# Optimization experiments

Measured on AMD Instinct MI355X. Metric: run time of the kernel, lower is better.

Reference implementation:

```python
import jax, jax.numpy as jnp
import numpy as np

HEADS = 8
DIM_HEAD = 64
DIM = 512
NUM_BANDS = 32
MAX_FREQ = 32.0
NORM_SCALE = 10.0
RPE_DIM = (NUM_BANDS * 2 + 1) * 2  # 130


def setup_inputs() -> dict:
    key = jax.random.key(0)
    ks = jax.random.split(key, 9)
    B, N = 2, 512
    inner = HEADS * DIM_HEAD
    h2 = HEADS * 2
    inp = {
        "x": jax.random.normal(ks[0], (B, N, DIM), dtype=jnp.float32),
        "positions": jax.random.uniform(ks[1], (B, N, 2), dtype=jnp.float32),
        "W_qkv": jax.random.normal(ks[2], (DIM, 3 * inner), dtype=jnp.float32) / np.sqrt(DIM),
        "W_out": jax.random.normal(ks[3], (inner, DIM), dtype=jnp.float32) / np.sqrt(inner),
        "b_out": jnp.zeros((DIM,), dtype=jnp.float32),
        "rpe_W1": jax.random.normal(ks[4], (RPE_DIM, h2), dtype=jnp.float32) / np.sqrt(RPE_DIM),
        "rpe_b1": jnp.zeros((h2,), dtype=jnp.float32),
        "rpe_W2": jax.random.normal(ks[5], (h2, HEADS), dtype=jnp.float32) / np.sqrt(h2),
        "rpe_b2": jnp.zeros((HEADS,), dtype=jnp.float32),
    }
    return inp


def _fourier_encode(x):
    # x: [...], returns [..., 2*NUM_BANDS+1]
    freqs = jnp.linspace(1.0, MAX_FREQ, NUM_BANDS, dtype=x.dtype)
    angles = x[..., None] * freqs * jnp.pi
    return jnp.concatenate([x[..., None], jnp.sin(angles), jnp.cos(angles)], axis=-1)


def _rpe_bias(positions, W1, b1, W2, b2):
    # positions: [B, N, 2] -> bias [B, H, N, N]
    delta = positions[:, None, :, :] - positions[:, :, None, :]  # key_pos_j - query_pos_i
    dx = delta[..., 0] / NORM_SCALE
    dy = delta[..., 1] / NORM_SCALE
    dx = dx / (1.0 + jnp.abs(dx))
    dy = dy / (1.0 + jnp.abs(dy))
    feats = jnp.concatenate([_fourier_encode(dx), _fourier_encode(dy)], axis=-1)  # [B,N,N,130]
    h = jax.nn.gelu(feats @ W1 + b1, approximate=False)
    bias = h @ W2 + b2  # [B, N, N, H]
    return jnp.transpose(bias, (0, 3, 1, 2))  # [B, H, N, N]


def reference(x, positions, W_qkv, W_out, b_out, rpe_W1, rpe_b1, rpe_W2, rpe_b2):
    B, N, _ = x.shape
    H, d = HEADS, DIM_HEAD
    scale = d ** (-0.5)
    qkv = x @ W_qkv  # [B, N, 3*H*d]
    q, k, v = jnp.split(qkv, 3, axis=-1)
    q = q.reshape(B, N, H, d)
    k = k.reshape(B, N, H, d)
    v = v.reshape(B, N, H, d)
    scores = jnp.einsum('bihd,bjhd->bhij', q, k) * scale
    scores = scores + _rpe_bias(positions, rpe_W1, rpe_b1, rpe_W2, rpe_b2)
    attn = jax.nn.softmax(scores, axis=-1)
    out = jnp.einsum('bhij,bjhd->bihd', attn, v).reshape(B, N, H * d)
    return out @ W_out + b_out
```

## Files before the change

### kernel.cpp

```cpp
#include <hip/hip_runtime.h>
#include <hip/hip_fp16.h>
#include <math.h>

typedef __attribute__((ext_vector_type(8))) _Float16 f16x8;
typedef __attribute__((ext_vector_type(4))) float f32x4;

#define TBL 512
#define UMAXV (1.0f/11.0f)

__device__ __forceinline__ int swq(int row, int q) {
  return row * 64 + ((q ^ (row & 7)) << 3);
}
__device__ __forceinline__ f16x8 cvt8(float4 a, float4 b) {
  f16x8 r;
  r[0] = (_Float16)a.x; r[1] = (_Float16)a.y;
  r[2] = (_Float16)a.z; r[3] = (_Float16)a.w;
  r[4] = (_Float16)b.x; r[5] = (_Float16)b.y;
  r[6] = (_Float16)b.z; r[7] = (_Float16)b.w;
  return r;
}

__global__ __launch_bounds__(256) void k_prep(
    const float* __restrict__ Wqkv, const float* __restrict__ Wout,
    const float* __restrict__ W1, const float* __restrict__ b1,
    _Float16* __restrict__ Wt, _Float16* __restrict__ Wot,
    __half* __restrict__ Tx, __half* __restrict__ Ty) {
  __shared__ float Tt[32 * 33];
  const int t = threadIdx.x;
  const int bid = blockIdx.x;
  if (bid >= 1024) {
    int gid = (bid - 1024) * 256 + t;
    int e = gid >> 5, c = gid & 31;
    float u = -UMAXV + (2.0f * UMAXV) * (float)e / (float)(TBL - 1);
    const int xpart = (c < 16);
    const int col = c & 15;
    const int base = xpart ? 0 : 65;
    float sum = u * W1[base * 16 + col] + (xpart ? b1[col] : 0.0f);
    float s1, c1;
    sincosf(u * 3.14159265358979323846f, &s1, &c1);
    float sk = s1, ck = c1;
    for (int k = 1; k <= 32; ++k) {
      sum += sk * W1[(base + k) * 16 + col] + ck * W1[(base + 32 + k) * 16 + col];
      float ns = sk * c1 + ck * s1;
      ck = ck * c1 - sk * s1;
      sk = ns;
    }
    (xpart ? Tx : Ty)[e * 16 + col] = __float2half(sum);
    return;
  }
  int k0, n0, ncols;
  const float* W;
  _Float16* O;
  if (bid < 768) {
    k0 = (bid / 48) * 32; n0 = (bid % 48) * 32; ncols = 1536;
    W = Wqkv; O = Wt;
  } else {
    int tile = bid - 768;
    k0 = (tile / 16) * 32; n0 = (tile % 16) * 32; ncols = 512;
    W = Wout; O = Wot;
  }
  {
    int kl = t >> 3, nl = (t & 7) * 4;
    float4 v = *(const float4*)&W[(k0 + kl) * ncols + n0 + nl];
    Tt[kl * 33 + nl + 0] = v.x;
    Tt[kl * 33 + nl + 1] = v.y;
    Tt[kl * 33 + nl + 2] = v.z;
    Tt[kl * 33 + nl + 3] = v.w;
  }
  __syncthreads();
  {
    int nl = t >> 3, kq = (t & 7) * 4;
    ushort4 h;
    h.x = __builtin_bit_cast(unsigned short, (_Float16)Tt[(kq + 0) * 33 + nl]);
    h.y = __builtin_bit_cast(unsigned short, (_Float16)Tt[(kq + 1) * 33 + nl]);
    h.z = __builtin_bit_cast(unsigned short, (_Float16)Tt[(kq + 2) * 33 + nl]);
    h.w = __builtin_bit_cast(unsigned short, (_Float16)Tt[(kq + 3) * 33 + nl]);
    *(ushort4*)&O[(n0 + nl) * 512 + k0 + kq] = h;
  }
}

__global__ __launch_bounds__(512) void k_fused(
    const float* __restrict__ x, const _Float16* __restrict__ Wt,
    _Float16* __restrict__ q16, _Float16* __restrict__ k16,
    _Float16* __restrict__ vt16,
    const float* __restrict__ pos,
    const __half* __restrict__ Tx, const __half* __restrict__ Ty,
    const float* __restrict__ W2, const float* __restrict__ b2,
    _Float16* __restrict__ bias) {
  __shared__ __align__(16) unsigned short SM[16384];
  const int bid = blockIdx.x;
  const int t = threadIdx.x;

  if (bid < 192) {
    _Float16* Ah = (_Float16*)SM;
    _Float16* Bh = (_Float16*)SM + 8192;
    const int mt = bid / 24, nt = bid % 24;
    const int m0 = mt * 128, n0 = nt * 64;
    const int w = t >> 6, lane = t & 63, blk = lane >> 4, jc = lane & 15;
    const int mw = (w & 3) * 32, nw = (w >> 2) * 32;
    const int sa = t >> 3, sq = t & 7;

    f32x4 acc[2][2];
    #pragma unroll
    for (int i = 0; i < 2; ++i)
      #pragma unroll
      for (int j = 0; j < 2; ++j) acc[i][j] = f32x4{0.f, 0.f, 0.f, 0.f};

    float4 pax[2][2];
    f16x8 pbv;
    #pragma unroll
    for (int c = 0; c < 2; ++c) {
      const float* xp = &x[(m0 + sa + c * 64) * 512 + sq * 8];
      pax[c][0] = *(const float4*)xp;
      pax[c][1] = *(const float4*)(xp + 4);
    }
    pbv = *(const f16x8*)&Wt[(n0 + sa) * 512 + sq * 8];

    for (int it = 0; it < 8; ++it) {
      #pragma unroll
      for (int c = 0; c < 2; ++c)
        *(f16x8*)&Ah[swq(sa + c * 64, sq)] = cvt8(pax[c][0], pax[c][1]);
      *(f16x8*)&Bh[swq(sa, sq)] = pbv;
      __syncthreads();
      if (it < 7) {
        int k0 = (it + 1) * 64;
        #pragma unroll
        for (int c = 0; c < 2; ++c) {
          const float* xp = &x[(m0 + sa + c * 64) * 512 + k0 + sq * 8];
          pax[c][0] = *(const float4*)xp;
          pax[c][1] = *(const float4*)(xp + 4);
        }
        pbv = *(const f16x8*)&Wt[(n0 + sa) * 512 + k0 + sq * 8];
      }
      #pragma unroll
      for (int h = 0; h < 2; ++h) {
        int q = h * 4 + blk;
        f16x8 a0 = *(const f16x8*)&Ah[swq(mw + jc, q)];
        f16x8 a1 = *(const f16x8*)&Ah[swq(mw + 16 + jc, q)];
        f16x8 b0 = *(const f16x8*)&Bh[swq(nw + jc, q)];
        f16x8 b1 = *(const f16x8*)&Bh[swq(nw + 16 + jc, q)];
        acc[0][0] = __builtin_amdgcn_mfma_f32_16x16x32_f16(a0, b0, acc[0][0], 0, 0, 0);
        acc[0][1] = __builtin_amdgcn_mfma_f32_16x16x32_f16(a0, b1, acc[0][1], 0, 0, 0);
        acc[1][0] = __builtin_amdgcn_mfma_f32_16x16x32_f16(a1, b0, acc[1][0], 0, 0, 0);
        acc[1][1] = __builtin_amdgcn_mfma_f32_16x16x32_f16(a1, b1, acc[1][1], 0, 0, 0);
      }
      __syncthreads();
    }
    const int sec = n0 >> 9;
    const int hh_ = (n0 >> 6) & 7;
    if (sec < 2) {
      _Float16* dst = (sec == 0) ? q16 : k16;
      const float scl = (sec == 0) ? 0.125f : 1.0f;
      #pragma unroll
      for (int i = 0; i < 2; ++i)
        #pragma unroll
        for (int j = 0; j < 2; ++j)
          #pragma unroll
          for (int r = 0; r < 4; ++r) {
            int tok = m0 + mw + i * 16 + blk * 4 + r;
            int b = tok >> 9, nn = tok & 511;
            int d = nw + j * 16 + jc;
            dst[((b * 8 + hh_) * 512 + nn) * 64 + d] = (_Float16)(acc[i][j][r] * scl);
          }
    } else {
      _Float16* T = (_Float16*)SM;
      #pragma unroll
      for (int i = 0; i < 2; ++i)
        #pragma unroll
        for (int j = 0; j < 2; ++j)
          #pragma unroll
          for (int r = 0; r < 4; ++r)
            T[(nw + j * 16 + jc) * 136 + mw + i * 16 + blk * 4 + r] =
                (_Float16)acc[i][j][r];
      __syncthreads();
      const int d = t >> 3, tq = t & 7;
      const int b = m0 >> 9, nb = m0 & 511;
      #pragma unroll
      for (int c = 0; c < 2; ++c) {
        int qd = tq + c * 8;
        f16x8 vv = *(const f16x8*)&T[d * 136 + qd * 8];
        *(f16x8*)&vt16[((b * 8 + hh_) * 64 + d) * 512 + nb + qd * 8] = vv;
      }
    }
    return;
  }

  const int gid = (bid - 192) * 512 + t;
  const int b = gid >> 18;
  const int i = (gid >> 9) & 511;
  const int j = gid & 511;
  const float pix = pos[(b * 512 + i) * 2 + 0];
  const float piy = pos[(b * 512 + i) * 2 + 1];
  const float pjx = pos[(b * 512 + j) * 2 + 0];
  const float pjy = pos[(b * 512 + j) * 2 + 1];
  float txv = (pjx - pix) * 0.1f; float ux = txv / (1.0f + fabsf(txv));
  float tyv = (pjy - piy) * 0.1f; float uy = tyv / (1.0f + fabsf(tyv));
  const float invstep = (float)(TBL - 1) / (2.0f * UMAXV);
  float fx = (ux + UMAXV) * invstep;
  int ix = (int)fx; ix = min(max(ix, 0), TBL - 2);
  float wx = fx - (float)ix;
  float fy = (uy + UMAXV) * invstep;
  int iy = (int)fy; iy = min(max(iy, 0), TBL - 2);
  float wy = fy - (float)iy;

  __half hx0[16], hx1[16], hy0[16], hy1[16];
  *(uint4*)&hx0[0] = *(const uint4*)&Tx[ix * 16];
  *(uint4*)&hx0[8] = *(const uint4*)&Tx[ix * 16 + 8];
  *(uint4*)&hx1[0] = *(const uint4*)&Tx[(ix + 1) * 16];
  *(uint4*)&hx1[8] = *(const uint4*)&Tx[(ix + 1) * 16 + 8];
  *(uint4*)&hy0[0] = *(const uint4*)&Ty[iy * 16];
  *(uint4*)&hy0[8] = *(const uint4*)&Ty[iy * 16 + 8];
  *(uint4*)&hy1[0] = *(const uint4*)&Ty[(iy + 1) * 16];
  *(uint4*)&hy1[8] = *(const uint4*)&Ty[(iy + 1) * 16 + 8];

  float o[8];
  #pragma unroll
  for (int c = 0; c < 8; ++c) o[c] = b2[c];
  #pragma unroll
  for (int r = 0; r < 16; ++r) {
    float ax = __half2float(hx0[r]);
    float bx = __half2float(hx1[r]);
    float ay = __half2float(hy0[r]);
    float by = __half2float(hy1[r]);
    float hv = fmaf(wx, bx - ax, ax) + fmaf(wy, by - ay, ay);
    float z = hv * 0.70710678118654752f;
    float az = fabsf(z);
    float tt = __builtin_amdgcn_rcpf(fmaf(0.3275911f, az, 1.0f));
    float poly = ((((1.061405429f * tt - 1.453152027f) * tt + 1.421413741f) * tt
                   - 0.284496736f) * tt + 0.254829592f) * tt;
    float ex = __expf(-z * z);
    float erfv = copysignf(fmaf(-poly, ex, 1.0f), z);
    float g = 0.5f * hv * (1.0f + erfv);
    #pragma unroll
    for (int c = 0; c < 8; ++c)
      o[c] = fmaf(g, W2[r * 8 + c], o[c]);
  }
  #pragma unroll
  for (int c = 0; c < 8; ++c)
    bias[((size_t)(b * 8 + c) * 512 + i) * 512 + j] = (_Float16)o[c];
}

__global__ __launch_bounds__(512) void k_attn(
    const _Float16* __restrict__ q16, const _Float16* __restrict__ k16,
    const _Float16* __restrict__ vt16, const _Float16* __restrict__ bias,
    _Float16* __restrict__ ao16) {
  __shared__ __align__(16) _Float16 psu[8 * 512];
  __shared__ __align__(16) float olds[8 * 16 * 65];
  __shared__ float mls[8 * 16 * 2];
  _Float16* bst = (_Float16*)olds;

  const int bid = blockIdx.x;
  const int it = bid & 31, h = (bid >> 5) & 7, b = bid >> 8;
  const int i0 = it * 16;
  const int bh = b * 8 + h;
  const int tid = threadIdx.x;
  const int w = tid >> 6, lane = tid & 63;
  const int blk = lane >> 4, jc = lane & 15;

  {
    const _Float16* bgp = bias + ((size_t)(bh * 512 + i0)) * 512;
    int brow = tid >> 5, bc = (tid & 31) * 16;
    *(f16x8*)&bst[brow * 520 + bc]     = *(const f16x8*)&bgp[brow * 512 + bc];
    *(f16x8*)&bst[brow * 520 + bc + 8] = *(const f16x8*)&bgp[brow * 512 + bc + 8];
  }

  const int qoff = (bh * 512 + i0 + jc) * 64 + blk * 8;
  const f16x8 qa0 = *(const f16x8*)&q16[qoff];
  const f16x8 qa1 = *(const f16x8*)&q16[qoff + 32];

  float m[4] = {-1e30f, -1e30f, -1e30f, -1e30f};
  float l[4] = {0.f, 0.f, 0.f, 0.f};
  f32x4 o[4];
  #pragma unroll
  for (int dt = 0; dt < 4; ++dt) o[dt] = f32x4{0.f, 0.f, 0.f, 0.f};

  _Float16* pw = &psu[w * 512];
  __syncthreads();

  #pragma unroll
  for (int jt = 0; jt < 2; ++jt) {
    const int j0 = w * 64 + jt * 32;
    const int rA = (bh * 512 + j0 + jc) * 64 + blk * 8;
    const int rB = rA + 16 * 64;
    f16x8 kA0 = *(const f16x8*)&k16[rA];
    f16x8 kA1 = *(const f16x8*)&k16[rA + 32];
    f16x8 kB0 = *(const f16x8*)&k16[rB];
    f16x8 kB1 = *(const f16x8*)&k16[rB + 32];

    f32x4 aA = {0.f, 0.f, 0.f, 0.f};
    aA = __builtin_amdgcn_mfma_f32_16x16x32_f16(qa0, kA0, aA, 0, 0, 0);
    aA = __builtin_amdgcn_mfma_f32_16x16x32_f16(qa1, kA1, aA, 0, 0, 0);
    f32x4 aB = {0.f, 0.f, 0.f, 0.f};
    aB = __builtin_amdgcn_mfma_f32_16x16x32_f16(qa0, kB0, aB, 0, 0, 0);
    aB = __builtin_amdgcn_mfma_f32_16x16x32_f16(qa1, kB1, aB, 0, 0, 0);

    float sA[4], sB[4], sc[4];
    #pragma unroll
    for (int r = 0; r < 4; ++r) {
      const int br = (blk * 4 + r) * 520;
      sA[r] = aA[r] + (float)bst[br + j0 + jc];
      sB[r] = aB[r] + (float)bst[br + j0 + 16 + jc];
    }
    #pragma unroll
    for (int r = 0; r < 4; ++r) {
      float mx = fmaxf(sA[r], sB[r]);
      mx = fmaxf(mx, __shfl_xor(mx, 1, 64));
      mx = fmaxf(mx, __shfl_xor(mx, 2, 64));
      mx = fmaxf(mx, __shfl_xor(mx, 4, 64));
      mx = fmaxf(mx, __shfl_xor(mx, 8, 64));
      float mn = fmaxf(m[r], mx);
      sc[r] = __expf(m[r] - mn);
      m[r] = mn;
      float pA = __expf(sA[r] - mn);
      float pB = __expf(sB[r] - mn);
      float ps = pA + pB;
      ps += __shfl_xor(ps, 1, 64);
      ps += __shfl_xor(ps, 2, 64);
      ps += __shfl_xor(ps, 4, 64);
      ps += __shfl_xor(ps, 8, 64);
      l[r] = l[r] * sc[r] + ps;
      pw[(blk * 4 + r) * 32 + jc] = (_Float16)pA;
      pw[(blk * 4 + r) * 32 + 16 + jc] = (_Float16)pB;
    }
    #pragma unroll
    for (int dt = 0; dt < 4; ++dt)
      #pragma unroll
      for (int r = 0; r < 4; ++r)
        o[dt][r] *= sc[r];
    f16x8 pf = *(const f16x8*)&pw[jc * 32 + blk * 8];
    #pragma unroll
    for (int dt = 0; dt < 4; ++dt) {
      const int va = (bh * 64 + dt * 16 + jc) * 512 + j0 + blk * 8;
      f16x8 vh = *(const f16x8*)&vt16[va];
      o[dt] = __builtin_amdgcn_mfma_f32_16x16x32_f16(pf, vh, o[dt], 0, 0, 0);
    }
  }
  __syncthreads();
  #pragma unroll
  for (int dt = 0; dt < 4; ++dt)
    #pragma unroll
    for (int r = 0; r < 4; ++r)
      olds[(w * 16 + blk * 4 + r) * 65 + dt * 16 + jc] = o[dt][r];
  if (jc == 0) {
    #pragma unroll
    for (int r = 0; r < 4; ++r) {
      mls[(w * 16 + blk * 4 + r) * 2 + 0] = m[r];
      mls[(w * 16 + blk * 4 + r) * 2 + 1] = l[r];
    }
  }
  __syncthreads();
  #pragma unroll
  for (int itx = 0; itx < 2; ++itx) {
    int idx = tid + itx * 512;
    int q = idx >> 6, d = idx & 63;
    float M = -1e30f;
    #pragma unroll
    for (int ww = 0; ww < 8; ++ww) M = fmaxf(M, mls[(ww * 16 + q) * 2]);
    float L = 0.f, acc = 0.f;
    #pragma unroll
    for (int ww = 0; ww < 8; ++ww) {
      float e = __expf(mls[(ww * 16 + q) * 2] - M);
      L += mls[(ww * 16 + q) * 2 + 1] * e;
      acc += olds[(ww * 16 + q) * 65 + d] * e;
    }
    ao16[(b * 512 + i0 + q) * 512 + h * 64 + d] = (_Float16)(acc / L);
  }
}

__global__ __launch_bounds__(256) void k_out(
    const _Float16* __restrict__ ao16, const _Float16* __restrict__ Wot,
    const float* __restrict__ bout, float* __restrict__ out) {
  __shared__ __align__(16) unsigned short SM[6144];
  _Float16* Ah = (_Float16*)SM;
  _Float16* Bh = (_Float16*)SM + 2048;

  const int bid = blockIdx.x;
  const int mt = bid >> 3, nt = bid & 7;
  const int m0 = mt * 32, n0 = nt * 64;
  const int t = threadIdx.x;
  const int w = t >> 6, lane = t & 63, blk = lane >> 4, jc = lane & 15;
  const int mh_ = (w & 1) * 16, nh_ = (w >> 1) * 32;
  const int sm = t >> 3, sq = t & 7;

  f32x4 acc[2];
  acc[0] = f32x4{0.f, 0.f, 0.f, 0.f};
  acc[1] = f32x4{0.f, 0.f, 0.f, 0.f};

  f16x8 pa, pb[2];
  {
    pa = *(const f16x8*)&ao16[(m0 + sm) * 512 + sq * 8];
    #pragma unroll
    for (int c = 0; c < 2; ++c)
      pb[c] = *(const f16x8*)&Wot[(n0 + sm + c * 32) * 512 + sq * 8];
  }
  for (int it = 0; it < 8; ++it) {
    *(f16x8*)&Ah[swq(sm, sq)] = pa;
    #pragma unroll
    for (int c = 0; c < 2; ++c)
      *(f16x8*)&Bh[swq(sm + c * 32, sq)] = pb[c];
    __syncthreads();
    if (it < 7) {
      int k0 = (it + 1) * 64;
      pa = *(const f16x8*)&ao16[(m0 + sm) * 512 + k0 + sq * 8];
      #pragma unroll
      for (int c = 0; c < 2; ++c)
        pb[c] = *(const f16x8*)&Wot[(n0 + sm + c * 32) * 512 + k0 + sq * 8];
    }
    #pragma unroll
    for (int h = 0; h < 2; ++h) {
      int q = h * 4 + blk;
      f16x8 a0 = *(const f16x8*)&Ah[swq(mh_ + jc, q)];
      f16x8 b0 = *(const f16x8*)&Bh[swq(nh_ + jc, q)];
      f16x8 b1 = *(const f16x8*)&Bh[swq(nh_ + 16 + jc, q)];
      acc[0] = __builtin_amdgcn_mfma_f32_16x16x32_f16(a0, b0, acc[0], 0, 0, 0);
      acc[1] = __builtin_amdgcn_mfma_f32_16x16x32_f16(a0, b1, acc[1], 0, 0, 0);
    }
    __syncthreads();
  }
  #pragma unroll
  for (int j = 0; j < 2; ++j) {
    int n = n0 + nh_ + j * 16 + jc;
    float bb = bout[n];
    #pragma unroll
    for (int r = 0; r < 4; ++r) {
      int row = m0 + mh_ + blk * 4 + r;
      out[row * 512 + n] = acc[j][r] + bb;
    }
  }
}

extern "C" void kernel_launch(void* const* d_in, const int* in_sizes, int n_in,
                              void* d_out, int out_size, void* d_ws, size_t ws_size,
                              hipStream_t stream) {
  const float* x    = (const float*)d_in[0];
  const float* pos  = (const float*)d_in[1];
  const float* Wqkv = (const float*)d_in[2];
  const float* Wout = (const float*)d_in[3];
  const float* bout = (const float*)d_in[4];
  const float* W1   = (const float*)d_in[5];
  const float* b1   = (const float*)d_in[6];
  const float* W2   = (const float*)d_in[7];
  const float* b2   = (const float*)d_in[8];
  float* out = (float*)d_out;
  char* base = (char*)d_ws;

  __half* Tx       = (__half*)(base);
  __half* Ty       = (__half*)(base + 16384);
  _Float16* Wt     = (_Float16*)(base + 32768);
  _Float16* Wot    = (_Float16*)(base + 1605632);
  _Float16* q16    = (_Float16*)(base + 2129920);
  _Float16* k16    = (_Float16*)(base + 3178496);
  _Float16* vt16   = (_Float16*)(base + 4227072);
  _Float16* bias16 = (_Float16*)(base + 5275648);
  _Float16* ao16   = (_Float16*)(base + 13664256);

  hipLaunchKernelGGL(k_prep, dim3(1088), dim3(256), 0, stream,
                     Wqkv, Wout, W1, b1, Wt, Wot, Tx, Ty);
  hipLaunchKernelGGL(k_fused, dim3(1216), dim3(512), 0, stream,
                     x, Wt, q16, k16, vt16, pos, Tx, Ty, W2, b2, bias16);
  hipLaunchKernelGGL(k_attn, dim3(512), dim3(512), 0, stream,
                     q16, k16, vt16, bias16, ao16);
  hipLaunchKernelGGL(k_out, dim3(256), dim3(256), 0, stream,
                     ao16, Wot, bout, out);
}
```

Before: 43.97 us.

## Prefetch all K-tiles into registers and double-buffer LDS in GEMM and attention kernels

The QKV projection and output-projection GEMMs now issue every global load for all eight K-steps up front into registers, then use two LDS buffers so only one barrier per step is needed. The attention kernel hoists all K and V fragment loads ahead of the softmax loop. The aim is to expose more memory-level parallelism and hide global load latency. In exchange, register pressure rises sharply (e.g. 32 float4 per thread in the fused kernel) and LDS use grows, which may lower occupancy or cause spills.

New measurement: 46.56 us. 1.06x slower.

```diff
diff --git a/kernel.cpp b/kernel.cpp
--- a/kernel.cpp
+++ b/kernel.cpp
@@ -87,13 +87,13 @@
     const __half* __restrict__ Tx, const __half* __restrict__ Ty,
     const float* __restrict__ W2, const float* __restrict__ b2,
     _Float16* __restrict__ bias) {
-  __shared__ __align__(16) unsigned short SM[16384];
+  __shared__ __align__(16) char SMEM[49152];
   const int bid = blockIdx.x;
   const int t = threadIdx.x;
 
   if (bid < 192) {
-    _Float16* Ah = (_Float16*)SM;
-    _Float16* Bh = (_Float16*)SM + 8192;
+    _Float16* Ah[2] = {(_Float16*)SMEM, (_Float16*)SMEM + 12288};
+    _Float16* Bh[2] = {(_Float16*)SMEM + 8192, (_Float16*)SMEM + 20480};
     const int mt = bid / 24, nt = bid % 24;
     const int m0 = mt * 128, n0 = nt * 64;
     const int w = t >> 6, lane = t & 63, blk = lane >> 4, jc = lane & 15;
@@ -106,39 +106,41 @@
       #pragma unroll
       for (int j = 0; j < 2; ++j) acc[i][j] = f32x4{0.f, 0.f, 0.f, 0.f};
 
-    float4 pax[2][2];
-    f16x8 pbv;
-    #pragma unroll
-    for (int c = 0; c < 2; ++c) {
-      const float* xp = &x[(m0 + sa + c * 64) * 512 + sq * 8];
-      pax[c][0] = *(const float4*)xp;
-      pax[c][1] = *(const float4*)(xp + 4);
-    }
-    pbv = *(const f16x8*)&Wt[(n0 + sa) * 512 + sq * 8];
-
+    float4 pax[8][2][2];
+    f16x8 pbv[8];
+    #pragma unroll
     for (int it = 0; it < 8; ++it) {
       #pragma unroll
-      for (int c = 0; c < 2; ++c)
-        *(f16x8*)&Ah[swq(sa + c * 64, sq)] = cvt8(pax[c][0], pax[c][1]);
-      *(f16x8*)&Bh[swq(sa, sq)] = pbv;
-      __syncthreads();
+      for (int c = 0; c < 2; ++c) {
+        const float* xp = &x[(m0 + sa + c * 64) * 512 + it * 64 + sq * 8];
+        pax[it][c][0] = *(const float4*)xp;
+        pax[it][c][1] = *(const float4*)(xp + 4);
+      }
+      pbv[it] = *(const f16x8*)&Wt[(n0 + sa) * 512 + it * 64 + sq * 8];
+    }
+    #pragma unroll
+    for (int c = 0; c < 2; ++c)
+      *(f16x8*)&Ah[0][swq(sa + c * 64, sq)] = cvt8(pax[0][c][0], pax[0][c][1]);
+    *(f16x8*)&Bh[0][swq(sa, sq)] = pbv[0];
+    __syncthreads();
+
+    #pragma unroll
+    for (int it = 0; it < 8; ++it) {
+      const int cur = it & 1, nxt = cur ^ 1;
       if (it < 7) {
-        int k0 = (it + 1) * 64;
         #pragma unroll
-        for (int c = 0; c < 2; ++c) {
-          const float* xp = &x[(m0 + sa + c * 64) * 512 + k0 + sq * 8];
-          pax[c][0] = *(const float4*)xp;
-          pax[c][1] = *(const float4*)(xp + 4);
-        }
-        pbv = *(const f16x8*)&Wt[(n0 + sa) * 512 + k0 + sq * 8];
+        for (int c = 0; c < 2; ++c)
+          *(f16x8*)&Ah[nxt][swq(sa + c * 64, sq)] =
+              cvt8(pax[it + 1][c][0], pax[it + 1][c][1]);
+        *(f16x8*)&Bh[nxt][swq(sa, sq)] = pbv[it + 1];
       }
       #pragma unroll
       for (int h = 0; h < 2; ++h) {
         int q = h * 4 + blk;
-        f16x8 a0 = *(const f16x8*)&Ah[swq(mw + jc, q)];
-        f16x8 a1 = *(const f16x8*)&Ah[swq(mw + 16 + jc, q)];
-        f16x8 b0 = *(const f16x8*)&Bh[swq(nw + jc, q)];
-        f16x8 b1 = *(const f16x8*)&Bh[swq(nw + 16 + jc, q)];
+        f16x8 a0 = *(const f16x8*)&Ah[cur][swq(mw + jc, q)];
+        f16x8 a1 = *(const f16x8*)&Ah[cur][swq(mw + 16 + jc, q)];
+        f16x8 b0 = *(const f16x8*)&Bh[cur][swq(nw + jc, q)];
+        f16x8 b1 = *(const f16x8*)&Bh[cur][swq(nw + 16 + jc, q)];
         acc[0][0] = __builtin_amdgcn_mfma_f32_16x16x32_f16(a0, b0, acc[0][0], 0, 0, 0);
         acc[0][1] = __builtin_amdgcn_mfma_f32_16x16x32_f16(a0, b1, acc[0][1], 0, 0, 0);
         acc[1][0] = __builtin_amdgcn_mfma_f32_16x16x32_f16(a1, b0, acc[1][0], 0, 0, 0);
@@ -163,7 +165,7 @@
             dst[((b * 8 + hh_) * 512 + nn) * 64 + d] = (_Float16)(acc[i][j][r] * scl);
           }
     } else {
-      _Float16* T = (_Float16*)SM;
+      _Float16* T = (_Float16*)SMEM;
       #pragma unroll
       for (int i = 0; i < 2; ++i)
         #pragma unroll
@@ -268,31 +270,39 @@
   const f16x8 qa0 = *(const f16x8*)&q16[qoff];
   const f16x8 qa1 = *(const f16x8*)&q16[qoff + 32];
 
-  float m[4] = {-1e30f, -1e30f, -1e30f, -1e30f};
-  float l[4] = {0.f, 0.f, 0.f, 0.f};
-  f32x4 o[4];
-  #pragma unroll
-  for (int dt = 0; dt < 4; ++dt) o[dt] = f32x4{0.f, 0.f, 0.f, 0.f};
-
-  _Float16* pw = &psu[w * 512];
-  __syncthreads();
-
+  f16x8 kf[2][4], vf[2][4];
   #pragma unroll
   for (int jt = 0; jt < 2; ++jt) {
     const int j0 = w * 64 + jt * 32;
     const int rA = (bh * 512 + j0 + jc) * 64 + blk * 8;
     const int rB = rA + 16 * 64;
-    f16x8 kA0 = *(const f16x8*)&k16[rA];
-    f16x8 kA1 = *(const f16x8*)&k16[rA + 32];
-    f16x8 kB0 = *(const f16x8*)&k16[rB];
-    f16x8 kB1 = *(const f16x8*)&k16[rB + 32];
-
+    kf[jt][0] = *(const f16x8*)&k16[rA];
+    kf[jt][1] = *(const f16x8*)&k16[rA + 32];
+    kf[jt][2] = *(const f16x8*)&k16[rB];
+    kf[jt][3] = *(const f16x8*)&k16[rB + 32];
+    #pragma unroll
+    for (int dt = 0; dt < 4; ++dt)
+      vf[jt][dt] = *(const f16x8*)&vt16[(bh * 64 + dt * 16 + jc) * 512 + j0 + blk * 8];
+  }
+
+  float m[4] = {-1e30f, -1e30f, -1e30f, -1e30f};
+  float l[4] = {0.f, 0.f, 0.f, 0.f};
+  f32x4 o[4];
+  #pragma unroll
+  for (int dt = 0; dt < 4; ++dt) o[dt] = f32x4{0.f, 0.f, 0.f, 0.f};
+
+  _Float16* pw = &psu[w * 512];
+  __syncthreads();
+
+  #pragma unroll
+  for (int jt = 0; jt < 2; ++jt) {
+    const int j0 = w * 64 + jt * 32;
     f32x4 aA = {0.f, 0.f, 0.f, 0.f};
-    aA = __builtin_amdgcn_mfma_f32_16x16x32_f16(qa0, kA0, aA, 0, 0, 0);
-    aA = __builtin_amdgcn_mfma_f32_16x16x32_f16(qa1, kA1, aA, 0, 0, 0);
+    aA = __builtin_amdgcn_mfma_f32_16x16x32_f16(qa0, kf[jt][0], aA, 0, 0, 0);
+    aA = __builtin_amdgcn_mfma_f32_16x16x32_f16(qa1, kf[jt][1], aA, 0, 0, 0);
     f32x4 aB = {0.f, 0.f, 0.f, 0.f};
-    aB = __builtin_amdgcn_mfma_f32_16x16x32_f16(qa0, kB0, aB, 0, 0, 0);
-    aB = __builtin_amdgcn_mfma_f32_16x16x32_f16(qa1, kB1, aB, 0, 0, 0);
+    aB = __builtin_amdgcn_mfma_f32_16x16x32_f16(qa0, kf[jt][2], aB, 0, 0, 0);
+    aB = __builtin_amdgcn_mfma_f32_16x16x32_f16(qa1, kf[jt][3], aB, 0, 0, 0);
 
     float sA[4], sB[4], sc[4];
     #pragma unroll
@@ -329,11 +339,8 @@
         o[dt][r] *= sc[r];
     f16x8 pf = *(const f16x8*)&pw[jc * 32 + blk * 8];
     #pragma unroll
-    for (int dt = 0; dt < 4; ++dt) {
-      const int va = (bh * 64 + dt * 16 + jc) * 512 + j0 + blk * 8;
-      f16x8 vh = *(const f16x8*)&vt16[va];
-      o[dt] = __builtin_amdgcn_mfma_f32_16x16x32_f16(pf, vh, o[dt], 0, 0, 0);
-    }
+    for (int dt = 0; dt < 4; ++dt)
+      o[dt] = __builtin_amdgcn_mfma_f32_16x16x32_f16(pf, vf[jt][dt], o[dt], 0, 0, 0);
   }
   __syncthreads();
   #pragma unroll
@@ -370,9 +377,9 @@
 __global__ __launch_bounds__(256) void k_out(
     const _Float16* __restrict__ ao16, const _Float16* __restrict__ Wot,
     const float* __restrict__ bout, float* __restrict__ out) {
-  __shared__ __align__(16) unsigned short SM[6144];
-  _Float16* Ah = (_Float16*)SM;
-  _Float16* Bh = (_Float16*)SM + 2048;
+  __shared__ __align__(16) char SMEM[24576];
+  _Float16* Ah[2] = {(_Float16*)SMEM, (_Float16*)SMEM + 6144};
+  _Float16* Bh[2] = {(_Float16*)SMEM + 2048, (_Float16*)SMEM + 8192};
 
   const int bid = blockIdx.x;
   const int mt = bid >> 3, nt = bid & 7;
@@ -386,32 +393,35 @@
   acc[0] = f32x4{0.f, 0.f, 0.f, 0.f};
   acc[1] = f32x4{0.f, 0.f, 0.f, 0.f};
 
-  f16x8 pa, pb[2];
-  {
-    pa = *(const f16x8*)&ao16[(m0 + sm) * 512 + sq * 8];
+  f16x8 pa[8], pb[8][2];
+  #pragma unroll
+  for (int it = 0; it < 8; ++it) {
+    pa[it] = *(const f16x8*)&ao16[(m0 + sm) * 512 + it * 64 + sq * 8];
     #pragma unroll
     for (int c = 0; c < 2; ++c)
-      pb[c] = *(const f16x8*)&Wot[(n0 + sm + c * 32) * 512 + sq * 8];
-  }
+      pb[it][c] = *(const f16x8*)&Wot[(n0 + sm + c * 32) * 512 + it * 64 + sq * 8];
+  }
+  *(f16x8*)&Ah[0][swq(sm, sq)] = pa[0];
+  #pragma unroll
+  for (int c = 0; c < 2; ++c)
+    *(f16x8*)&Bh[0][swq(sm + c * 32, sq)] = pb[0][c];
+  __syncthreads();
+
+  #pragma unroll
   for (int it = 0; it < 8; ++it) {
-    *(f16x8*)&Ah[swq(sm, sq)] = pa;
-    #pragma unroll
-    for (int c = 0; c < 2; ++c)
-      *(f16x8*)&Bh[swq(sm + c * 32, sq)] = pb[c];
-    __syncthreads();
+    const int cur = it & 1, nxt = cur ^ 1;
     if (it < 7) {
-      int k0 = (it + 1) * 64;
-      pa = *(const f16x8*)&ao16[(m0 + sm) * 512 + k0 + sq * 8];
+      *(f16x8*)&Ah[nxt][swq(sm, sq)] = pa[it + 1];
       #pragma unroll
       for (int c = 0; c < 2; ++c)
-        pb[c] = *(const f16x8*)&Wot[(n0 + sm + c * 32) * 512 + k0 + sq * 8];
+        *(f16x8*)&Bh[nxt][swq(sm + c * 32, sq)] = pb[it + 1][c];
     }
     #pragma unroll
     for (int h = 0; h < 2; ++h) {
       int q = h * 4 + blk;
-      f16x8 a0 = *(const f16x8*)&Ah[swq(mh_ + jc, q)];
-      f16x8 b0 = *(const f16x8*)&Bh[swq(nh_ + jc, q)];
-      f16x8 b1 = *(const f16x8*)&Bh[swq(nh_ + 16 + jc, q)];
+      f16x8 a0 = *(const f16x8*)&Ah[cur][swq(mh_ + jc, q)];
+      f16x8 b0 = *(const f16x8*)&Bh[cur][swq(nh_ + jc, q)];
+      f16x8 b1 = *(const f16x8*)&Bh[cur][swq(nh_ + 16 + jc, q)];
       acc[0] = __builtin_amdgcn_mfma_f32_16x16x32_f16(a0, b0, acc[0], 0, 0, 0);
       acc[1] = __builtin_amdgcn_mfma_f32_16x16x32_f16(a0, b1, acc[1], 0, 0, 0);
     }
```

## Fuse attention with output projection, one wave per head over full key range

Applied to the files above, without the earlier changes.

Replaces the separate attention and output-projection kernels with one kernel. Each block now handles a 16-query tile for all 8 heads, one wave per head, and each wave loops over all 512 keys itself, so the cross-wave softmax merge is gone. The normalized head outputs are kept in swizzled shared memory and multiplied by W_out in the same block, which removes the ao16 round trip through global memory and one launch. The cost is a grid of only 64 blocks on a many-CU GPU and a longer serial key loop per wave, so parallelism drops sharply.

After: 72.35 us. 64.5% more time.

```diff
diff --git a/kernel.cpp b/kernel.cpp
--- a/kernel.cpp
+++ b/kernel.cpp
@@ -240,29 +240,22 @@
     bias[((size_t)(b * 8 + c) * 512 + i) * 512 + j] = (_Float16)o[c];
 }
 
-__global__ __launch_bounds__(512) void k_attn(
+__global__ __launch_bounds__(512) void k_attn2(
     const _Float16* __restrict__ q16, const _Float16* __restrict__ k16,
     const _Float16* __restrict__ vt16, const _Float16* __restrict__ bias,
-    _Float16* __restrict__ ao16) {
+    const _Float16* __restrict__ Wot, const float* __restrict__ bout,
+    float* __restrict__ out) {
   __shared__ __align__(16) _Float16 psu[8 * 512];
-  __shared__ __align__(16) float olds[8 * 16 * 65];
-  __shared__ float mls[8 * 16 * 2];
-  _Float16* bst = (_Float16*)olds;
+  __shared__ __align__(16) _Float16 bstw[8 * 512];
+  __shared__ __align__(16) _Float16 aos[16 * 512];
 
   const int bid = blockIdx.x;
-  const int it = bid & 31, h = (bid >> 5) & 7, b = bid >> 8;
+  const int it = bid & 31, b = bid >> 5;
   const int i0 = it * 16;
-  const int bh = b * 8 + h;
   const int tid = threadIdx.x;
   const int w = tid >> 6, lane = tid & 63;
   const int blk = lane >> 4, jc = lane & 15;
-
-  {
-    const _Float16* bgp = bias + ((size_t)(bh * 512 + i0)) * 512;
-    int brow = tid >> 5, bc = (tid & 31) * 16;
-    *(f16x8*)&bst[brow * 520 + bc]     = *(const f16x8*)&bgp[brow * 512 + bc];
-    *(f16x8*)&bst[brow * 520 + bc + 8] = *(const f16x8*)&bgp[brow * 512 + bc + 8];
-  }
+  const int bh = b * 8 + w;
 
   const int qoff = (bh * 512 + i0 + jc) * 64 + blk * 8;
   const f16x8 qa0 = *(const f16x8*)&q16[qoff];
@@ -275,11 +268,14 @@
   for (int dt = 0; dt < 4; ++dt) o[dt] = f32x4{0.f, 0.f, 0.f, 0.f};
 
   _Float16* pw = &psu[w * 512];
-  __syncthreads();
-
-  #pragma unroll
-  for (int jt = 0; jt < 2; ++jt) {
-    const int j0 = w * 64 + jt * 32;
+  _Float16* bw = &bstw[w * 512];
+  const int brow = lane >> 2, bcol = (lane & 3) * 8;
+  const _Float16* bgp = bias + ((size_t)(bh * 512 + i0)) * 512;
+
+  for (int js = 0; js < 16; ++js) {
+    const int j0 = js * 32;
+    *(f16x8*)&bw[brow * 32 + bcol] = *(const f16x8*)&bgp[brow * 512 + j0 + bcol];
+
     const int rA = (bh * 512 + j0 + jc) * 64 + blk * 8;
     const int rB = rA + 16 * 64;
     f16x8 kA0 = *(const f16x8*)&k16[rA];
@@ -297,9 +293,9 @@
     float sA[4], sB[4], sc[4];
     #pragma unroll
     for (int r = 0; r < 4; ++r) {
-      const int br = (blk * 4 + r) * 520;
-      sA[r] = aA[r] + (float)bst[br + j0 + jc];
-      sB[r] = aB[r] + (float)bst[br + j0 + 16 + jc];
+      const int br = (blk * 4 + r) * 32;
+      sA[r] = aA[r] + (float)bw[br + jc];
+      sB[r] = aB[r] + (float)bw[br + 16 + jc];
     }
     #pragma unroll
     for (int r = 0; r < 4; ++r) {
@@ -330,101 +326,46 @@
     f16x8 pf = *(const f16x8*)&pw[jc * 32 + blk * 8];
     #pragma unroll
     for (int dt = 0; dt < 4; ++dt) {
-      const int va = (bh * 64 + dt * 16 + jc) * 512 + j0 + blk * 8;
-      f16x8 vh = *(const f16x8*)&vt16[va];
+      const f16x8 vh = *(const f16x8*)&vt16[(bh * 64 + dt * 16 + jc) * 512 + j0 + blk * 8];
       o[dt] = __builtin_amdgcn_mfma_f32_16x16x32_f16(pf, vh, o[dt], 0, 0, 0);
     }
   }
+
+  float inv[4];
+  #pragma unroll
+  for (int r = 0; r < 4; ++r) inv[r] = 1.0f / l[r];
+  #pragma unroll
+  for (int dt = 0; dt < 4; ++dt)
+    #pragma unroll
+    for (int r = 0; r < 4; ++r) {
+      int row = blk * 4 + r;
+      int col = w * 64 + dt * 16 + jc;
+      aos[row * 512 + (((col >> 3) ^ (row & 7)) << 3) + (col & 7)] =
+          (_Float16)(o[dt][r] * inv[r]);
+    }
   __syncthreads();
-  #pragma unroll
-  for (int dt = 0; dt < 4; ++dt)
-    #pragma unroll
-    for (int r = 0; r < 4; ++r)
-      olds[(w * 16 + blk * 4 + r) * 65 + dt * 16 + jc] = o[dt][r];
-  if (jc == 0) {
+
+  f32x4 acc[4];
+  #pragma unroll
+  for (int ns = 0; ns < 4; ++ns) acc[ns] = f32x4{0.f, 0.f, 0.f, 0.f};
+  #pragma unroll
+  for (int ks = 0; ks < 16; ++ks) {
+    const f16x8 af = *(const f16x8*)&aos[jc * 512 + (((ks * 4 + blk) ^ (jc & 7)) << 3)];
+    #pragma unroll
+    for (int ns = 0; ns < 4; ++ns) {
+      const f16x8 bf =
+          *(const f16x8*)&Wot[(w * 64 + ns * 16 + jc) * 512 + ks * 32 + blk * 8];
+      acc[ns] = __builtin_amdgcn_mfma_f32_16x16x32_f16(af, bf, acc[ns], 0, 0, 0);
+    }
+  }
+  #pragma unroll
+  for (int ns = 0; ns < 4; ++ns) {
+    int n = w * 64 + ns * 16 + jc;
+    float bb = bout[n];
     #pragma unroll
     for (int r = 0; r < 4; ++r) {
-      mls[(w * 16 + blk * 4 + r) * 2 + 0] = m[r];
-      mls[(w * 16 + blk * 4 + r) * 2 + 1] = l[r];
-    }
-  }
-  __syncthreads();
-  #pragma unroll
-  for (int itx = 0; itx < 2; ++itx) {
-    int idx = tid + itx * 512;
-    int q = idx >> 6, d = idx & 63;
-    float M = -1e30f;
-    #pragma unroll
-    for (int ww = 0; ww < 8; ++ww) M = fmaxf(M, mls[(ww * 16 + q) * 2]);
-    float L = 0.f, acc = 0.f;
-    #pragma unroll
-    for (int ww = 0; ww < 8; ++ww) {
-      float e = __expf(mls[(ww * 16 + q) * 2] - M);
-      L += mls[(ww * 16 + q) * 2 + 1] * e;
-      acc += olds[(ww * 16 + q) * 65 + d] * e;
-    }
-    ao16[(b * 512 + i0 + q) * 512 + h * 64 + d] = (_Float16)(acc / L);
-  }
-}
-
-__global__ __launch_bounds__(256) void k_out(
-    const _Float16* __restrict__ ao16, const _Float16* __restrict__ Wot,
-    const float* __restrict__ bout, float* __restrict__ out) {
-  __shared__ __align__(16) unsigned short SM[6144];
-  _Float16* Ah = (_Float16*)SM;
-  _Float16* Bh = (_Float16*)SM + 2048;
-
-  const int bid = blockIdx.x;
-  const int mt = bid >> 3, nt = bid & 7;
-  const int m0 = mt * 32, n0 = nt * 64;
-  const int t = threadIdx.x;
-  const int w = t >> 6, lane = t & 63, blk = lane >> 4, jc = lane & 15;
-  const int mh_ = (w & 1) * 16, nh_ = (w >> 1) * 32;
-  const int sm = t >> 3, sq = t & 7;
-
-  f32x4 acc[2];
-  acc[0] = f32x4{0.f, 0.f, 0.f, 0.f};
-  acc[1] = f32x4{0.f, 0.f, 0.f, 0.f};
-
-  f16x8 pa, pb[2];
-  {
-    pa = *(const f16x8*)&ao16[(m0 + sm) * 512 + sq * 8];
-    #pragma unroll
-    for (int c = 0; c < 2; ++c)
-      pb[c] = *(const f16x8*)&Wot[(n0 + sm + c * 32) * 512 + sq * 8];
-  }
-  for (int it = 0; it < 8; ++it) {
-    *(f16x8*)&Ah[swq(sm, sq)] = pa;
-    #pragma unroll
-    for (int c = 0; c < 2; ++c)
-      *(f16x8*)&Bh[swq(sm + c * 32, sq)] = pb[c];
-    __syncthreads();
-    if (it < 7) {
-      int k0 = (it + 1) * 64;
-      pa = *(const f16x8*)&ao16[(m0 + sm) * 512 + k0 + sq * 8];
-      #pragma unroll
-      for (int c = 0; c < 2; ++c)
-        pb[c] = *(const f16x8*)&Wot[(n0 + sm + c * 32) * 512 + k0 + sq * 8];
-    }
-    #pragma unroll
-    for (int h = 0; h < 2; ++h) {
-      int q = h * 4 + blk;
-      f16x8 a0 = *(const f16x8*)&Ah[swq(mh_ + jc, q)];
-      f16x8 b0 = *(const f16x8*)&Bh[swq(nh_ + jc, q)];
-      f16x8 b1 = *(const f16x8*)&Bh[swq(nh_ + 16 + jc, q)];
-      acc[0] = __builtin_amdgcn_mfma_f32_16x16x32_f16(a0, b0, acc[0], 0, 0, 0);
-      acc[1] = __builtin_amdgcn_mfma_f32_16x16x32_f16(a0, b1, acc[1], 0, 0, 0);
-    }
-    __syncthreads();
-  }
-  #pragma unroll
-  for (int j = 0; j < 2; ++j) {
-    int n = n0 + nh_ + j * 16 + jc;
-    float bb = bout[n];
-    #pragma unroll
-    for (int r = 0; r < 4; ++r) {
-      int row = m0 + mh_ + blk * 4 + r;
-      out[row * 512 + n] = acc[j][r] + bb;
+      int row = i0 + blk * 4 + r;
+      out[(b * 512 + row) * 512 + n] = acc[ns][r] + bb;
     }
   }
 }
@@ -452,14 +393,11 @@
   _Float16* k16    = (_Float16*)(base + 3178496);
   _Float16* vt16   = (_Float16*)(base + 4227072);
   _Float16* bias16 = (_Float16*)(base + 5275648);
-  _Float16* ao16   = (_Float16*)(base + 13664256);
 
   hipLaunchKernelGGL(k_prep, dim3(1088), dim3(256), 0, stream,
                      Wqkv, Wout, W1, b1, Wt, Wot, Tx, Ty);
   hipLaunchKernelGGL(k_fused, dim3(1216), dim3(512), 0, stream,
                      x, Wt, q16, k16, vt16, pos, Tx, Ty, W2, b2, bias16);
-  hipLaunchKernelGGL(k_attn, dim3(512), dim3(512), 0, stream,
-                     q16, k16, vt16, bias16, ao16);
-  hipLaunchKernelGGL(k_out, dim3(256), dim3(256), 0, stream,
-                     ao16, Wot, bout, out);
-}
+  hipLaunchKernelGGL(k_attn2, dim3(64), dim3(512), 0, stream,
+                     q16, k16, vt16, bias16, Wot, bout, out);
+}
```

## Deepen register prefetch to two stages and remap block order for XCD locality

Applied to the files above, without the earlier changes.

The QKV GEMM and output-projection GEMM now prefetch two k-tiles ahead into registers instead of one, aiming to hide global load latency. The attention kernel's two-tile loop is unrolled by hand so the K and V loads for both tiles are issued early, ahead of the MFMA and softmax work. All three kernels remap blockIdx so consecutive logical tiles are spread across groups of eight, presumably to place related tiles on the same XCD for L2 reuse. The cost is higher register pressure, which may lower occupancy.

Measured after the change: 43.14 us, median of 2. Within noise of the previous version (-1.9%).

```diff
diff --git a/kernel.cpp b/kernel.cpp
--- a/kernel.cpp
+++ b/kernel.cpp
@@ -92,9 +92,10 @@
   const int t = threadIdx.x;
 
   if (bid < 192) {
+    const int gb = (bid & 7) * 24 + (bid >> 3);
     _Float16* Ah = (_Float16*)SM;
     _Float16* Bh = (_Float16*)SM + 8192;
-    const int mt = bid / 24, nt = bid % 24;
+    const int mt = gb / 24, nt = gb % 24;
     const int m0 = mt * 128, n0 = nt * 64;
     const int w = t >> 6, lane = t & 63, blk = lane >> 4, jc = lane & 15;
     const int mw = (w & 3) * 32, nw = (w >> 2) * 32;
@@ -106,31 +107,35 @@
       #pragma unroll
       for (int j = 0; j < 2; ++j) acc[i][j] = f32x4{0.f, 0.f, 0.f, 0.f};
 
-    float4 pax[2][2];
-    f16x8 pbv;
-    #pragma unroll
-    for (int c = 0; c < 2; ++c) {
-      const float* xp = &x[(m0 + sa + c * 64) * 512 + sq * 8];
-      pax[c][0] = *(const float4*)xp;
-      pax[c][1] = *(const float4*)(xp + 4);
-    }
-    pbv = *(const f16x8*)&Wt[(n0 + sa) * 512 + sq * 8];
+    float4 pax[2][2][2];
+    f16x8 pbv[2];
+    #pragma unroll
+    for (int s = 0; s < 2; ++s) {
+      #pragma unroll
+      for (int c = 0; c < 2; ++c) {
+        const float* xp = &x[(m0 + sa + c * 64) * 512 + s * 64 + sq * 8];
+        pax[s][c][0] = *(const float4*)xp;
+        pax[s][c][1] = *(const float4*)(xp + 4);
+      }
+      pbv[s] = *(const f16x8*)&Wt[(n0 + sa) * 512 + s * 64 + sq * 8];
+    }
 
     for (int it = 0; it < 8; ++it) {
+      const int slot = it & 1;
       #pragma unroll
       for (int c = 0; c < 2; ++c)
-        *(f16x8*)&Ah[swq(sa + c * 64, sq)] = cvt8(pax[c][0], pax[c][1]);
-      *(f16x8*)&Bh[swq(sa, sq)] = pbv;
+        *(f16x8*)&Ah[swq(sa + c * 64, sq)] = cvt8(pax[slot][c][0], pax[slot][c][1]);
+      *(f16x8*)&Bh[swq(sa, sq)] = pbv[slot];
       __syncthreads();
-      if (it < 7) {
-        int k0 = (it + 1) * 64;
+      if (it < 6) {
+        int k0 = (it + 2) * 64;
         #pragma unroll
         for (int c = 0; c < 2; ++c) {
           const float* xp = &x[(m0 + sa + c * 64) * 512 + k0 + sq * 8];
-          pax[c][0] = *(const float4*)xp;
-          pax[c][1] = *(const float4*)(xp + 4);
+          pax[slot][c][0] = *(const float4*)xp;
+          pax[slot][c][1] = *(const float4*)(xp + 4);
         }
-        pbv = *(const f16x8*)&Wt[(n0 + sa) * 512 + k0 + sq * 8];
+        pbv[slot] = *(const f16x8*)&Wt[(n0 + sa) * 512 + k0 + sq * 8];
       }
       #pragma unroll
       for (int h = 0; h < 2; ++h) {
@@ -249,8 +254,8 @@
   __shared__ float mls[8 * 16 * 2];
   _Float16* bst = (_Float16*)olds;
 
-  const int bid = blockIdx.x;
-  const int it = bid & 31, h = (bid >> 5) & 7, b = bid >> 8;
+  const int lb = (blockIdx.x & 7) * 64 + (blockIdx.x >> 3);
+  const int it = lb & 31, h = (lb >> 5) & 7, b = lb >> 8;
   const int i0 = it * 16;
   const int bh = b * 8 + h;
   const int tid = threadIdx.x;
@@ -268,6 +273,20 @@
   const f16x8 qa0 = *(const f16x8*)&q16[qoff];
   const f16x8 qa1 = *(const f16x8*)&q16[qoff + 32];
 
+  const int j00 = w * 64;
+  f16x8 k0A0, k0A1, k0B0, k0B1, v0[4];
+  {
+    const int rA = (bh * 512 + j00 + jc) * 64 + blk * 8;
+    const int rB = rA + 16 * 64;
+    k0A0 = *(const f16x8*)&k16[rA];
+    k0A1 = *(const f16x8*)&k16[rA + 32];
+    k0B0 = *(const f16x8*)&k16[rB];
+    k0B1 = *(const f16x8*)&k16[rB + 32];
+    #pragma unroll
+    for (int dt = 0; dt < 4; ++dt)
+      v0[dt] = *(const f16x8*)&vt16[(bh * 64 + dt * 16 + jc) * 512 + j00 + blk * 8];
+  }
+
   float m[4] = {-1e30f, -1e30f, -1e30f, -1e30f};
   float l[4] = {0.f, 0.f, 0.f, 0.f};
   f32x4 o[4];
@@ -277,29 +296,34 @@
   _Float16* pw = &psu[w * 512];
   __syncthreads();
 
-  #pragma unroll
-  for (int jt = 0; jt < 2; ++jt) {
-    const int j0 = w * 64 + jt * 32;
-    const int rA = (bh * 512 + j0 + jc) * 64 + blk * 8;
+  f32x4 aA = {0.f, 0.f, 0.f, 0.f};
+  aA = __builtin_amdgcn_mfma_f32_16x16x32_f16(qa0, k0A0, aA, 0, 0, 0);
+  aA = __builtin_amdgcn_mfma_f32_16x16x32_f16(qa1, k0A1, aA, 0, 0, 0);
+  f32x4 aB = {0.f, 0.f, 0.f, 0.f};
+  aB = __builtin_amdgcn_mfma_f32_16x16x32_f16(qa0, k0B0, aB, 0, 0, 0);
+  aB = __builtin_amdgcn_mfma_f32_16x16x32_f16(qa1, k0B1, aB, 0, 0, 0);
+
+  const int j01 = w * 64 + 32;
+  f16x8 k1A0, k1A1, k1B0, k1B1, v1[4];
+  {
+    const int rA = (bh * 512 + j01 + jc) * 64 + blk * 8;
     const int rB = rA + 16 * 64;
-    f16x8 kA0 = *(const f16x8*)&k16[rA];
-    f16x8 kA1 = *(const f16x8*)&k16[rA + 32];
-    f16x8 kB0 = *(const f16x8*)&k16[rB];
-    f16x8 kB1 = *(const f16x8*)&k16[rB + 32];
-
-    f32x4 aA = {0.f, 0.f, 0.f, 0.f};
-    aA = __builtin_amdgcn_mfma_f32_16x16x32_f16(qa0, kA0, aA, 0, 0, 0);
-    aA = __builtin_amdgcn_mfma_f32_16x16x32_f16(qa1, kA1, aA, 0, 0, 0);
-    f32x4 aB = {0.f, 0.f, 0.f, 0.f};
-    aB = __builtin_amdgcn_mfma_f32_16x16x32_f16(qa0, kB0, aB, 0, 0, 0);
-    aB = __builtin_amdgcn_mfma_f32_16x16x32_f16(qa1, kB1, aB, 0, 0, 0);
-
+    k1A0 = *(const f16x8*)&k16[rA];
+    k1A1 = *(const f16x8*)&k16[rA + 32];
+    k1B0 = *(const f16x8*)&k16[rB];
+    k1B1 = *(const f16x8*)&k16[rB + 32];
+    #pragma unroll
+    for (int dt = 0; dt < 4; ++dt)
+      v1[dt] = *(const f16x8*)&vt16[(bh * 64 + dt * 16 + jc) * 512 + j01 + blk * 8];
+  }
+
+  {
     float sA[4], sB[4], sc[4];
     #pragma unroll
     for (int r = 0; r < 4; ++r) {
       const int br = (blk * 4 + r) * 520;
-      sA[r] = aA[r] + (float)bst[br + j0 + jc];
-      sB[r] = aB[r] + (float)bst[br + j0 + 16 + jc];
+      sA[r] = aA[r] + (float)bst[br + j00 + jc];
+      sB[r] = aB[r] + (float)bst[br + j00 + 16 + jc];
     }
     #pragma unroll
     for (int r = 0; r < 4; ++r) {
@@ -329,12 +353,56 @@
         o[dt][r] *= sc[r];
     f16x8 pf = *(const f16x8*)&pw[jc * 32 + blk * 8];
     #pragma unroll
-    for (int dt = 0; dt < 4; ++dt) {
-      const int va = (bh * 64 + dt * 16 + jc) * 512 + j0 + blk * 8;
-      f16x8 vh = *(const f16x8*)&vt16[va];
-      o[dt] = __builtin_amdgcn_mfma_f32_16x16x32_f16(pf, vh, o[dt], 0, 0, 0);
-    }
-  }
+    for (int dt = 0; dt < 4; ++dt)
+      o[dt] = __builtin_amdgcn_mfma_f32_16x16x32_f16(pf, v0[dt], o[dt], 0, 0, 0);
+  }
+
+  aA = f32x4{0.f, 0.f, 0.f, 0.f};
+  aA = __builtin_amdgcn_mfma_f32_16x16x32_f16(qa0, k1A0, aA, 0, 0, 0);
+  aA = __builtin_amdgcn_mfma_f32_16x16x32_f16(qa1, k1A1, aA, 0, 0, 0);
+  aB = f32x4{0.f, 0.f, 0.f, 0.f};
+  aB = __builtin_amdgcn_mfma_f32_16x16x32_f16(qa0, k1B0, aB, 0, 0, 0);
+  aB = __builtin_amdgcn_mfma_f32_16x16x32_f16(qa1, k1B1, aB, 0, 0, 0);
+  {
+    float sA[4], sB[4], sc[4];
+    #pragma unroll
+    for (int r = 0; r < 4; ++r) {
+      const int br = (blk * 4 + r) * 520;
+      sA[r] = aA[r] + (float)bst[br + j01 + jc];
+      sB[r] = aB[r] + (float)bst[br + j01 + 16 + jc];
+    }
+    #pragma unroll
+    for (int r = 0; r < 4; ++r) {
+      float mx = fmaxf(sA[r], sB[r]);
+      mx = fmaxf(mx, __shfl_xor(mx, 1, 64));
+      mx = fmaxf(mx, __shfl_xor(mx, 2, 64));
+      mx = fmaxf(mx, __shfl_xor(mx, 4, 64));
+      mx = fmaxf(mx, __shfl_xor(mx, 8, 64));
+      float mn = fmaxf(m[r], mx);
+      sc[r] = __expf(m[r] - mn);
+      m[r] = mn;
+      float pA = __expf(sA[r] - mn);
+      float pB = __expf(sB[r] - mn);
+      float ps = pA + pB;
+      ps += __shfl_xor(ps, 1, 64);
+      ps += __shfl_xor(ps, 2, 64);
+      ps += __shfl_xor(ps, 4, 64);
+      ps += __shfl_xor(ps, 8, 64);
+      l[r] = l[r] * sc[r] + ps;
+      pw[(blk * 4 + r) * 32 + jc] = (_Float16)pA;
+      pw[(blk * 4 + r) * 32 + 16 + jc] = (_Float16)pB;
+    }
+    #pragma unroll
+    for (int dt = 0; dt < 4; ++dt)
+      #pragma unroll
+      for (int r = 0; r < 4; ++r)
+        o[dt][r] *= sc[r];
+    f16x8 pf = *(const f16x8*)&pw[jc * 32 + blk * 8];
+    #pragma unroll
+    for (int dt = 0; dt < 4; ++dt)
+      o[dt] = __builtin_amdgcn_mfma_f32_16x16x32_f16(pf, v1[dt], o[dt], 0, 0, 0);
+  }
+
   __syncthreads();
   #pragma unroll
   for (int dt = 0; dt < 4; ++dt)
@@ -374,8 +442,8 @@
   _Float16* Ah = (_Float16*)SM;
   _Float16* Bh = (_Float16*)SM + 2048;
 
-  const int bid = blockIdx.x;
-  const int mt = bid >> 3, nt = bid & 7;
+  const int lb = (blockIdx.x & 7) * 32 + (blockIdx.x >> 3);
+  const int mt = lb >> 3, nt = lb & 7;
   const int m0 = mt * 32, n0 = nt * 64;
   const int t = threadIdx.x;
   const int w = t >> 6, lane = t & 63, blk = lane >> 4, jc = lane & 15;
@@ -386,25 +454,27 @@
   acc[0] = f32x4{0.f, 0.f, 0.f, 0.f};
   acc[1] = f32x4{0.f, 0.f, 0.f, 0.f};
 
-  f16x8 pa, pb[2];
-  {
-    pa = *(const f16x8*)&ao16[(m0 + sm) * 512 + sq * 8];
+  f16x8 pa[2], pb[2][2];
+  #pragma unroll
+  for (int s = 0; s < 2; ++s) {
+    pa[s] = *(const f16x8*)&ao16[(m0 + sm) * 512 + s * 64 + sq * 8];
     #pragma unroll
     for (int c = 0; c < 2; ++c)
-      pb[c] = *(const f16x8*)&Wot[(n0 + sm + c * 32) * 512 + sq * 8];
+      pb[s][c] = *(const f16x8*)&Wot[(n0 + sm + c * 32) * 512 + s * 64 + sq * 8];
   }
   for (int it = 0; it < 8; ++it) {
-    *(f16x8*)&Ah[swq(sm, sq)] = pa;
+    const int slot = it & 1;
+    *(f16x8*)&Ah[swq(sm, sq)] = pa[slot];
     #pragma unroll
     for (int c = 0; c < 2; ++c)
-      *(f16x8*)&Bh[swq(sm + c * 32, sq)] = pb[c];
+      *(f16x8*)&Bh[swq(sm + c * 32, sq)] = pb[slot][c];
     __syncthreads();
-    if (it < 7) {
-      int k0 = (it + 1) * 64;
-      pa = *(const f16x8*)&ao16[(m0 + sm) * 512 + k0 + sq * 8];
+    if (it < 6) {
+      int k0 = (it + 2) * 64;
+      pa[slot] = *(const f16x8*)&ao16[(m0 + sm) * 512 + k0 + sq * 8];
       #pragma unroll
       for (int c = 0; c < 2; ++c)
-        pb[c] = *(const f16x8*)&Wot[(n0 + sm + c * 32) * 512 + k0 + sq * 8];
+        pb[slot][c] = *(const f16x8*)&Wot[(n0 + sm + c * 32) * 512 + k0 + sq * 8];
     }
     #pragma unroll
     for (int h = 0; h < 2; ++h) {
```
